# Kernel tuning notes

Hardware: AMD Instinct MI355X
Metric: run time of the kernel (lower is better)

## Reference

```python
import jax, jax.numpy as jnp
import numpy as np

N, K, C, CL = 1024, 32, 64, 128
H = 2 * C  # MLP hidden = 2 * pair channels


def _ln(x, g, b, eps=1e-5):
    m = x.mean(-1, keepdims=True)
    v = jnp.mean(jnp.square(x - m), -1, keepdims=True)
    return (x - m) * jax.lax.rsqrt(v + eps) * g + b


def setup_inputs() -> dict:
    key = jax.random.key(0)
    ks = jax.random.split(key, 16)

    def w(k, shape):
        return jax.random.normal(k, shape, jnp.float32) / np.float32(np.sqrt(shape[0]))

    local = jax.random.normal(ks[0], (N, CL), jnp.float32)
    pair = jax.random.normal(ks[1], (N, N, C), jnp.float32)
    pair_update = jax.random.normal(ks[2], (N, K, C), jnp.float32)
    r = jax.random.randint(ks[3], (N, K), -(N // 4), N)
    neighbours = jnp.where(r < 0, -1, r)
    mask = jax.random.bernoulli(ks[4], 0.9, (N,))
    return dict(
        local=local, pair=pair, pair_update=pair_update,
        neighbours=neighbours, mask=mask,
        Wa=w(ks[5], (CL, C)), Wb=w(ks[6], (CL, C)),
        ln_g=jnp.ones((C,), jnp.float32), ln_b=jnp.zeros((C,), jnp.float32),
        W_aug=w(ks[7], (C, C)), W_lin=w(ks[8], (C, C)),
        W_left=w(ks[9], (C, 32)), b_left=jnp.zeros((32,), jnp.float32),
        W_right=w(ks[10], (C, 32)), b_right=jnp.zeros((32,), jnp.float32),
        W1=w(ks[11], (32, H)), W2=w(ks[12], (H, C)),
        W_int=w(ks[13], (CL, C)), b_int=jnp.zeros((C,), jnp.float32),
    )


def reference(local, pair, pair_update, neighbours, mask,
              Wa, Wb, ln_g, ln_b, W_aug, W_lin,
              W_left, b_left, W_right, b_right, W1, W2, W_int, b_int):
    idx = jnp.arange(pair.shape[0])
    # inject local info into the sparse pair update   [N,K,C]
    pu = pair_update + (local @ Wa)[:, None] + (local @ Wb)[neighbours]
    # gather neighbour pair features + layernorm      [N,K,C]
    lp = _ln(pair[idx[:, None], neighbours], ln_g, ln_b)
    lp = lp + pu @ W_aug
    linear = lp @ W_lin                               # [N,K,C]
    left = lp @ W_left + b_left                       # [N,K,32]
    right = lp @ W_right + b_right                    # [N,K,32]
    # neighbour-of-neighbour pair features            [N,K,K,32]
    npair = left[:, None] + right[neighbours]
    pn = neighbours[neighbours]                       # [N,K,K]
    pn = jnp.where((neighbours == -1)[:, :, None], pn, -1)
    pm = (pn != -1) & mask[pn] & (neighbours != -1)[:, None, :]
    # fused per-edge-pair MLP                          [N,K,K,C]
    upd = jax.nn.gelu(npair @ W1) @ W2
    # masked mean over the middle neighbour axis       [N,K,C]
    upd = jnp.where(pm[..., None], upd, 0.0).sum(axis=1)
    upd = upd / jnp.maximum(pm.sum(axis=1), 1).astype(upd.dtype)[..., None]
    inter = local @ W_int + b_int                     # [N,C]
    # scatter-add back into the dense pair tensor (collisions possible)
    return pair.at[idx[:, None], neighbours].add(upd + inter[:, None] + linear)
```

## Files before the change

### kernel.cpp

```cpp
#include <hip/hip_runtime.h>
#include <hip/hip_bf16.h>

constexpr int Nn  = 1024;
constexpr int Kk  = 32;
constexpr int Cc  = 64;
constexpr int CLl = 128;

typedef unsigned int   u32;
typedef unsigned short u16;
typedef float f4v __attribute__((ext_vector_type(4)));

__device__ __forceinline__ float gelu_tanh(float v){
  float c = 0.7978845608028654f*(v + 0.044715f*v*v*v);
  return 0.5f*v*(1.f + tanhf(c));
}
__device__ __forceinline__ float bflo(u32 u){ return __uint_as_float(u<<16); }
__device__ __forceinline__ float bfhi(u32 u){ return __uint_as_float(u & 0xffff0000u); }
__device__ __forceinline__ u32 pack_bf(float a, float b){
  u32 xa = __float_as_uint(a), xb = __float_as_uint(b);
  u32 ra = (xa + 0x7fffu + ((xa>>16)&1u)) >> 16;
  u32 rb = (xb + 0x7fffu + ((xb>>16)&1u)) >> 16;
  return ra | (rb<<16);
}

__global__ __launch_bounds__(256) void kcopy(
    const f4v* __restrict__ src, f4v* __restrict__ dst,
    const float* __restrict__ local, const float* __restrict__ Wa,
    const float* __restrict__ Wb, const float* __restrict__ Wint,
    const float* __restrict__ b_int,
    float* __restrict__ A, float* __restrict__ B, float* __restrict__ inter){
  const int tid = threadIdx.x;
  size_t base = (size_t)blockIdx.x * (256*32) + tid;
  #pragma unroll
  for(int g = 0; g < 4; ++g){
    f4v v[8];
    #pragma unroll
    for(int j = 0; j < 8; ++j)
      v[j] = __builtin_nontemporal_load(&src[base + (size_t)(g*8 + j)*256]);
    #pragma unroll
    for(int j = 0; j < 8; ++j)
      __builtin_nontemporal_store(v[j], &dst[base + (size_t)(g*8 + j)*256]);
  }
  if(blockIdx.x < (unsigned)Nn){
    __shared__ float l[CLl];
    if(tid < CLl) l[tid] = local[blockIdx.x*CLl + tid];
    __syncthreads();
    if(tid < 64){
      const int c = tid, i = blockIdx.x;
      float a = 0.f, b = 0.f, t = 0.f;
      #pragma unroll 4
      for(int d = 0; d < CLl; ++d){
        float ld = l[d];
        a = fmaf(ld, Wa[d*Cc + c], a);
        b = fmaf(ld, Wb[d*Cc + c], b);
        t = fmaf(ld, Wint[d*Cc + c], t);
      }
      A[i*Cc + c] = a;
      B[i*Cc + c] = b;
      inter[i*Cc + c] = t + b_int[c];
    }
  }
}

__global__ __launch_bounds__(256) void k1(
    const float* __restrict__ pair, const float* __restrict__ pair_update,
    const int* __restrict__ neigh, const int* __restrict__ mask,
    const float* __restrict__ ln_g, const float* __restrict__ ln_b,
    const float* __restrict__ W_aug, const float* __restrict__ W_right,
    const float* __restrict__ b_right,
    const float* __restrict__ A, const float* __restrict__ B,
    float* __restrict__ r1023, int* __restrict__ qpart){
  const int i = Nn - 1;
  __shared__ float wA[4096];
  __shared__ float wR[2048];
  __shared__ float p [Kk][68];
  __shared__ float pu[Kk][68];
  __shared__ float lp[Kk][68];
  __shared__ int   nwS[Kk];
  __shared__ float ssum[Kk][9], ssq[Kk][9], stats[Kk][2];
  int tid = threadIdx.x;
  for(int idx = tid; idx < 4096; idx += 256) wA[idx] = W_aug[idx];
  for(int idx = tid; idx < 2048; idx += 256) wR[idx] = W_right[idx];
  if(tid < Kk){
    int n = neigh[i*Kk + tid];
    nwS[tid] = (n < 0) ? n + Nn : n;
    qpart[tid] = (n != -1 && mask[n] != 0) ? 1 : 0;
  }
  __syncthreads();
  int k = tid >> 3, s = tid & 7;
  {
    const float* prow = pair + ((size_t)i*Nn + nwS[k])*Cc + s*8;
    const float* pur  = pair_update + ((size_t)i*Kk + k)*Cc + s*8;
    const float* Ar = A + i*Cc + s*8;
    const float* Br = B + (size_t)nwS[k]*Cc + s*8;
    float ps = 0.f, ps2 = 0.f;
    for(int j = 0; j < 8; ++j){
      float v = prow[j];
      p[k][s*8 + j] = v; ps += v; ps2 += v*v;
      pu[k][s*8 + j] = pur[j] + Ar[j] + Br[j];
    }
    ssum[k][s] = ps; ssq[k][s] = ps2;
  }
  __syncthreads();
  if(s == 0){
    float m = 0.f, q = 0.f;
    for(int j = 0; j < 8; ++j){ m += ssum[k][j]; q += ssq[k][j]; }
    m *= (1.f/64.f); q *= (1.f/64.f);
    float var = fmaxf(q - m*m, 0.f);
    stats[k][0] = m; stats[k][1] = rsqrtf(var + 1e-5f);
  }
  __syncthreads();
  {
    float m = stats[k][0], r = stats[k][1];
    float acc[8];
    #pragma unroll
    for(int j = 0; j < 8; ++j){
      int c = s*8 + j;
      acc[j] = (p[k][c] - m)*r*ln_g[c] + ln_b[c];
    }
    for(int d = 0; d < 64; ++d){
      float pd = pu[k][d];
      #pragma unroll
      for(int j = 0; j < 8; ++j) acc[j] = fmaf(pd, wA[d*64 + s*8 + j], acc[j]);
    }
    #pragma unroll
    for(int j = 0; j < 8; ++j) lp[k][s*8 + j] = acc[j];
  }
  __syncthreads();
  {
    float acc[4] = {0.f,0.f,0.f,0.f};
    for(int d = 0; d < 64; ++d){
      float ld = lp[k][d];
      #pragma unroll
      for(int j = 0; j < 4; ++j) acc[j] = fmaf(ld, wR[d*32 + s*4 + j], acc[j]);
    }
    #pragma unroll
    for(int j = 0; j < 4; ++j)
      r1023[k*32 + s*4 + j] = acc[j] + b_right[s*4 + j];
  }
}

__global__ __launch_bounds__(256) void kcomp(
    const float* __restrict__ pair, const float* __restrict__ pair_update,
    const int* __restrict__ neigh,
    const float* __restrict__ ln_g, const float* __restrict__ ln_b,
    const float* __restrict__ W_aug, const float* __restrict__ W_lin,
    const float* __restrict__ W_left, const float* __restrict__ b_left,
    const float* __restrict__ W1, const float* __restrict__ W2,
    const float* __restrict__ A, const float* __restrict__ B,
    const float* __restrict__ inter, const float* __restrict__ r1023,
    const int* __restrict__ qpart,
    float* __restrict__ out){

  __shared__ u32 wbA[2048];
  __shared__ u32 wbL[2048];
  __shared__ u32 wbF[1024];
  __shared__ u32 w1b[2048];
  __shared__ u32 w2b[4096];
  __shared__ float pbuf[Kk][68];
  __shared__ u32  puP [Kk][34];
  __shared__ float uA[1088];
  __shared__ float stats[Kk][2];
  __shared__ float AiS[64], InS[64], lgS[64], lbS[64];
  __shared__ int nbS[Kk], nwS[Kk], quS[Kk], leadS[Kk];
  __shared__ int cminus;

  float* ssum = uA;
  float* ssq  = uA + 288;
  float* hbuf = uA;

  const int i   = blockIdx.x;
  const int tid = threadIdx.x;

  for(int idx = tid; idx < 2048; idx += 256){
    const float2 wa = *(const float2*)(W_aug + idx*2);
    wbA[idx] = pack_bf(wa.x, wa.y);
    const float2 wl = *(const float2*)(W_lin + idx*2);
    wbL[idx] = pack_bf(wl.x, wl.y);
    const float2 w1 = *(const float2*)(W1 + idx*2);
    w1b[idx] = pack_bf(w1.x, w1.y);
    const float2 w2a = *(const float2*)(W2 + idx*2);
    w2b[idx] = pack_bf(w2a.x, w2a.y);
    const float2 w2c = *(const float2*)(W2 + 4096 + idx*2);
    w2b[2048 + idx] = pack_bf(w2c.x, w2c.y);
  }
  for(int idx = tid; idx < 1024; idx += 256){
    const float2 wf = *(const float2*)(W_left + idx*2);
    wbF[idx] = pack_bf(wf.x, wf.y);
  }
  if(tid < Kk){
    int n = neigh[i*Kk + tid];
    nbS[tid] = n;
    nwS[tid] = (n < 0) ? n + Nn : n;
    quS[tid] = qpart[tid];
  }
  if(tid < 64){
    AiS[tid] = A[i*Cc + tid];
    InS[tid] = inter[i*Cc + tid];
    lgS[tid] = ln_g[tid];
    lbS[tid] = ln_b[tid];
  }
  __syncthreads();

  if(tid == 0){
    int c = 0;
    for(int kk = 0; kk < Kk; ++kk) c |= (nbS[kk] == -1);
    cminus = c;
  }
  if(tid < Kk){
    int lead = 1;
    for(int kk = 0; kk < tid; ++kk) if(nwS[kk] == nwS[tid]) lead = 0;
    leadS[tid] = lead;
  }

  float pf[8];
  {
    int k8 = tid >> 3, s8 = tid & 7;
    const float4* p4 = (const float4*)(pair + ((size_t)i*Nn + nwS[k8])*Cc) + s8*2;
    float4 p0 = p4[0], p1 = p4[1];
    const float4* u4 = (const float4*)(pair_update + ((size_t)i*Kk + k8)*Cc) + s8*2;
    float4 u0 = u4[0], u1 = u4[1];
    const float4* Br = (const float4*)(B + (size_t)nwS[k8]*Cc) + s8*2;
    float4 b0 = Br[0], b1 = Br[1];
    pf[0]=p0.x; pf[1]=p0.y; pf[2]=p0.z; pf[3]=p0.w;
    pf[4]=p1.x; pf[5]=p1.y; pf[6]=p1.z; pf[7]=p1.w;
    float uf[8] = {u0.x,u0.y,u0.z,u0.w,u1.x,u1.y,u1.z,u1.w};
    float bv[8] = {b0.x,b0.y,b0.z,b0.w,b1.x,b1.y,b1.z,b1.w};
    float ps = 0.f, ps2 = 0.f;
    #pragma unroll
    for(int j = 0; j < 8; ++j){
      float v = pf[j];
      pbuf[k8][s8*8 + j] = v; ps += v; ps2 += v*v;
    }
    #pragma unroll
    for(int j = 0; j < 4; ++j){
      float e0 = uf[2*j]   + AiS[s8*8 + 2*j]   + bv[2*j];
      float e1 = uf[2*j+1] + AiS[s8*8 + 2*j+1] + bv[2*j+1];
      puP[k8][s8*4 + j] = pack_bf(e0, e1);
    }
    ssum[k8*9 + s8] = ps; ssq[k8*9 + s8] = ps2;
  }
  __syncthreads();

  if((tid & 7) == 0){
    int k8 = tid >> 3;
    float m = 0.f, q = 0.f;
    for(int j = 0; j < 8; ++j){ m += ssum[k8*9 + j]; q += ssq[k8*9 + j]; }
    m *= (1.f/64.f); q *= (1.f/64.f);
    float var = fmaxf(q - m*m, 0.f);
    stats[k8][0] = m; stats[k8][1] = rsqrtf(var + 1e-5f);
  }
  __syncthreads();

  const int kq  = tid >> 4;
  const int s   = tid & 15;
  const int k0i = kq, k1i = kq + 16;
  const int c0  = s*4;

  float a0[4], a1[4];
  {
    float m0 = stats[k0i][0], r0 = stats[k0i][1];
    float m1 = stats[k1i][0], r1 = stats[k1i][1];
    #pragma unroll
    for(int j = 0; j < 4; ++j){
      int c = c0 + j;
      a0[j] = (pbuf[k0i][c] - m0)*r0*lgS[c] + lbS[c];
      a1[j] = (pbuf[k1i][c] - m1)*r1*lgS[c] + lbS[c];
    }
    #pragma unroll 2
    for(int dp = 0; dp < 32; ++dp){
      u32 q0 = puP[k0i][dp], q1 = puP[k1i][dp];
      float pe0 = bflo(q0), po0 = bfhi(q0);
      float pe1 = bflo(q1), po1 = bfhi(q1);
      uint2 we = *(const uint2*)&wbA[(2*dp)*32 + s*2];
      uint2 wo = *(const uint2*)&wbA[(2*dp+1)*32 + s*2];
      float w0 = bflo(we.x), w1 = bfhi(we.x), w2 = bflo(we.y), w3 = bfhi(we.y);
      a0[0] = fmaf(pe0, w0, a0[0]); a0[1] = fmaf(pe0, w1, a0[1]);
      a0[2] = fmaf(pe0, w2, a0[2]); a0[3] = fmaf(pe0, w3, a0[3]);
      a1[0] = fmaf(pe1, w0, a1[0]); a1[1] = fmaf(pe1, w1, a1[1]);
      a1[2] = fmaf(pe1, w2, a1[2]); a1[3] = fmaf(pe1, w3, a1[3]);
      float x0w = bflo(wo.x), x1w = bfhi(wo.x), x2w = bflo(wo.y), x3w = bfhi(wo.y);
      a0[0] = fmaf(po0, x0w, a0[0]); a0[1] = fmaf(po0, x1w, a0[1]);
      a0[2] = fmaf(po0, x2w, a0[2]); a0[3] = fmaf(po0, x3w, a0[3]);
      a1[0] = fmaf(po1, x0w, a1[0]); a1[1] = fmaf(po1, x1w, a1[1]);
      a1[2] = fmaf(po1, x2w, a1[2]); a1[3] = fmaf(po1, x3w, a1[3]);
    }
  }
  __syncthreads();
  #pragma unroll
  for(int j = 0; j < 4; ++j){ pbuf[k0i][c0 + j] = a0[j]; pbuf[k1i][c0 + j] = a1[j]; }
  __syncthreads();

  float L0[4], L1[4];
  {
    float Lx0[4] = {0,0,0,0}, Lx1[4] = {0,0,0,0};
    float X0[2] = {0,0}, X1[2] = {0,0};
    #pragma unroll 4
    for(int d = 0; d < 64; ++d){
      float p0 = pbuf[k0i][d], p1 = pbuf[k1i][d];
      uint2 wv = *(const uint2*)&wbL[d*32 + s*2];
      float w0 = bflo(wv.x), w1 = bfhi(wv.x), w2 = bflo(wv.y), w3 = bfhi(wv.y);
      Lx0[0] = fmaf(p0, w0, Lx0[0]); Lx0[1] = fmaf(p0, w1, Lx0[1]);
      Lx0[2] = fmaf(p0, w2, Lx0[2]); Lx0[3] = fmaf(p0, w3, Lx0[3]);
      Lx1[0] = fmaf(p1, w0, Lx1[0]); Lx1[1] = fmaf(p1, w1, Lx1[1]);
      Lx1[2] = fmaf(p1, w2, Lx1[2]); Lx1[3] = fmaf(p1, w3, Lx1[3]);
      u32 wf = wbF[d*16 + s];
      float f0 = bflo(wf), f1 = bfhi(wf);
      X0[0] = fmaf(p0, f0, X0[0]); X0[1] = fmaf(p0, f1, X0[1]);
      X1[0] = fmaf(p1, f0, X1[0]); X1[1] = fmaf(p1, f1, X1[1]);
    }
    #pragma unroll
    for(int j = 0; j < 4; ++j){
      L0[j] = Lx0[j] + InS[c0 + j];
      L1[j] = Lx1[j] + InS[c0 + j];
    }
    int x0 = s*2;
    float2 bl = *(const float2*)(b_left + x0);
    float2 rA = *(const float2*)(r1023 + k0i*32 + x0);
    float2 rB = *(const float2*)(r1023 + k1i*32 + x0);
    hbuf[k0i*34 + x0]     = X0[0] + bl.x + rA.x;
    hbuf[k0i*34 + x0 + 1] = X0[1] + bl.y + rA.y;
    hbuf[k1i*34 + x0]     = X1[0] + bl.x + rB.x;
    hbuf[k1i*34 + x0 + 1] = X1[1] + bl.y + rB.y;
  }
  __syncthreads();

  float g0[8], g1v[8];
  {
    float A0[8] = {0,0,0,0,0,0,0,0}, A1[8] = {0,0,0,0,0,0,0,0};
    #pragma unroll 2
    for(int x = 0; x < 32; ++x){
      float h0 = hbuf[k0i*34 + x], h1 = hbuf[k1i*34 + x];
      uint4 wv = *(const uint4*)&w1b[x*64 + s*4];
      float w[8] = {bflo(wv.x),bfhi(wv.x),bflo(wv.y),bfhi(wv.y),
                    bflo(wv.z),bfhi(wv.z),bflo(wv.w),bfhi(wv.w)};
      #pragma unroll
      for(int j = 0; j < 8; ++j){
        A0[j] = fmaf(h0, w[j], A0[j]);
        A1[j] = fmaf(h1, w[j], A1[j]);
      }
    }
    #pragma unroll
    for(int j = 0; j < 8; ++j){ g0[j] = gelu_tanh(A0[j]); g1v[j] = gelu_tanh(A1[j]); }
  }
  {
    float V0[4] = {0,0,0,0}, V1[4] = {0,0,0,0};
    int lbase = (kq & 3) << 4;
    for(int hb = 0; hb < 16; ++hb){
      int srcl = lbase | hb;
      #pragma unroll
      for(int hj = 0; hj < 8; ++hj){
        float gA = __shfl(g0[hj],  srcl, 64);
        float gB = __shfl(g1v[hj], srcl, 64);
        int h = hb*8 + hj;
        uint2 wv = *(const uint2*)&w2b[h*32 + s*2];
        float w0 = bflo(wv.x), w1 = bfhi(wv.x), w2 = bflo(wv.y), w3 = bfhi(wv.y);
        V0[0] = fmaf(gA, w0, V0[0]); V0[1] = fmaf(gA, w1, V0[1]);
        V0[2] = fmaf(gA, w2, V0[2]); V0[3] = fmaf(gA, w3, V0[3]);
        V1[0] = fmaf(gB, w0, V1[0]); V1[1] = fmaf(gB, w1, V1[1]);
        V1[2] = fmaf(gB, w2, V1[2]); V1[3] = fmaf(gB, w3, V1[3]);
      }
    }
    float mul0 = (cminus && quS[k0i] && nbS[k0i] != -1) ? 1.f : 0.f;
    float mul1 = (cminus && quS[k1i] && nbS[k1i] != -1) ? 1.f : 0.f;
    #pragma unroll
    for(int j = 0; j < 4; ++j){
      pbuf[k0i][c0 + j] = fmaf(mul0, V0[j], L0[j]);
      pbuf[k1i][c0 + j] = fmaf(mul1, V1[j], L1[j]);
    }
  }
  __syncthreads();

  {
    int k8 = tid >> 3, s8 = tid & 7;
    if(leadS[k8]){
      int col = nwS[k8];
      float tot[8] = {0,0,0,0,0,0,0,0};
      for(int kk = 0; kk < Kk; ++kk){
        if(nwS[kk] == col){
          #pragma unroll
          for(int j = 0; j < 8; ++j) tot[j] += pbuf[kk][s8*8 + j];
        }
      }
      size_t base = ((size_t)i*Nn + col)*Cc + s8*8;
      float4 o0 = make_float4(pf[0]+tot[0], pf[1]+tot[1], pf[2]+tot[2], pf[3]+tot[3]);
      float4 o1 = make_float4(pf[4]+tot[4], pf[5]+tot[5], pf[6]+tot[6], pf[7]+tot[7]);
      float4* ov = (float4*)(out + base);
      ov[0] = o0; ov[1] = o1;
    }
  }
}

extern "C" void kernel_launch(void* const* d_in, const int* in_sizes, int n_in,
                              void* d_out, int out_size, void* d_ws, size_t ws_size,
                              hipStream_t stream){
  (void)in_sizes; (void)n_in; (void)out_size; (void)ws_size;
  const float* local       = (const float*)d_in[0];
  const float* pair        = (const float*)d_in[1];
  const float* pair_update = (const float*)d_in[2];
  const int*   neighbours  = (const int*)d_in[3];
  const int*   mask        = (const int*)d_in[4];
  const float* Wa          = (const float*)d_in[5];
  const float* Wb          = (const float*)d_in[6];
  const float* ln_g        = (const float*)d_in[7];
  const float* ln_b        = (const float*)d_in[8];
  const float* W_aug       = (const float*)d_in[9];
  const float* W_lin       = (const float*)d_in[10];
  const float* W_left      = (const float*)d_in[11];
  const float* b_left      = (const float*)d_in[12];
  const float* W_right     = (const float*)d_in[13];
  const float* b_right     = (const float*)d_in[14];
  const float* W1          = (const float*)d_in[15];
  const float* W2          = (const float*)d_in[16];
  const float* W_int       = (const float*)d_in[17];
  const float* b_int       = (const float*)d_in[18];

  float* ws    = (float*)d_ws;
  float* A     = ws;
  float* B     = ws + 65536;
  float* inter = ws + 131072;
  float* r1023 = ws + 196608;
  int*   qpart = (int*)(ws + 197632);

  kcopy<<<dim3(2048), dim3(256), 0, stream>>>(
      (const f4v*)pair, (f4v*)d_out,
      local, Wa, Wb, W_int, b_int, A, B, inter);
  k1<<<dim3(1), dim3(256), 0, stream>>>(pair, pair_update, neighbours, mask,
                                        ln_g, ln_b, W_aug, W_right, b_right,
                                        A, B, r1023, qpart);
  kcomp<<<dim3(Nn), dim3(256), 0, stream>>>(pair, pair_update, neighbours,
                                            ln_g, ln_b, W_aug, W_lin,
                                            W_left, b_left, W1, W2,
                                            A, B, inter, r1023, qpart,
                                            (float*)d_out);
}
```

Before: 540.5 us.

## Alias kcomp weight LDS buffers for occupancy and split copy kernel

Result: slower. 558.4 us (+3.3%).

```diff
diff --git a/kernel.cpp b/kernel.cpp
--- a/kernel.cpp
+++ b/kernel.cpp
@@ -23,43 +23,28 @@
   return ra | (rb<<16);
 }
 
-__global__ __launch_bounds__(256) void kcopy(
-    const f4v* __restrict__ src, f4v* __restrict__ dst,
+__global__ __launch_bounds__(64) void k0(
     const float* __restrict__ local, const float* __restrict__ Wa,
     const float* __restrict__ Wb, const float* __restrict__ Wint,
     const float* __restrict__ b_int,
     float* __restrict__ A, float* __restrict__ B, float* __restrict__ inter){
-  const int tid = threadIdx.x;
-  size_t base = (size_t)blockIdx.x * (256*32) + tid;
-  #pragma unroll
-  for(int g = 0; g < 4; ++g){
-    f4v v[8];
-    #pragma unroll
-    for(int j = 0; j < 8; ++j)
-      v[j] = __builtin_nontemporal_load(&src[base + (size_t)(g*8 + j)*256]);
-    #pragma unroll
-    for(int j = 0; j < 8; ++j)
-      __builtin_nontemporal_store(v[j], &dst[base + (size_t)(g*8 + j)*256]);
-  }
-  if(blockIdx.x < (unsigned)Nn){
-    __shared__ float l[CLl];
-    if(tid < CLl) l[tid] = local[blockIdx.x*CLl + tid];
-    __syncthreads();
-    if(tid < 64){
-      const int c = tid, i = blockIdx.x;
-      float a = 0.f, b = 0.f, t = 0.f;
-      #pragma unroll 4
-      for(int d = 0; d < CLl; ++d){
-        float ld = l[d];
-        a = fmaf(ld, Wa[d*Cc + c], a);
-        b = fmaf(ld, Wb[d*Cc + c], b);
-        t = fmaf(ld, Wint[d*Cc + c], t);
-      }
-      A[i*Cc + c] = a;
-      B[i*Cc + c] = b;
-      inter[i*Cc + c] = t + b_int[c];
-    }
-  }
+  int i = blockIdx.x;
+  int c = threadIdx.x;
+  __shared__ float l[CLl];
+  l[c]      = local[i*CLl + c];
+  l[c + 64] = local[i*CLl + 64 + c];
+  __syncthreads();
+  float a = 0.f, b = 0.f, t = 0.f;
+  #pragma unroll 4
+  for(int d = 0; d < CLl; ++d){
+    float ld = l[d];
+    a = fmaf(ld, Wa[d*Cc + c], a);
+    b = fmaf(ld, Wb[d*Cc + c], b);
+    t = fmaf(ld, Wint[d*Cc + c], t);
+  }
+  A[i*Cc + c] = a;
+  B[i*Cc + c] = b;
+  inter[i*Cc + c] = t + b_int[c];
 }
 
 __global__ __launch_bounds__(256) void k1(
@@ -140,7 +125,21 @@
   }
 }
 
-__global__ __launch_bounds__(256) void kcomp(
+__global__ __launch_bounds__(256) void kcopy(
+    const f4v* __restrict__ src, f4v* __restrict__ dst){
+  const int tid = threadIdx.x;
+  size_t base = (size_t)blockIdx.x * (256*32) + tid;
+  #pragma unroll
+  for(int g = 0; g < 4; ++g){
+    f4v v[8];
+    #pragma unroll
+    for(int j = 0; j < 8; ++j) v[j] = src[base + (size_t)(g*8 + j)*256];
+    #pragma unroll
+    for(int j = 0; j < 8; ++j) dst[base + (size_t)(g*8 + j)*256] = v[j];
+  }
+}
+
+__global__ __launch_bounds__(256, 3) void kcomp(
     const float* __restrict__ pair, const float* __restrict__ pair_update,
     const int* __restrict__ neigh,
     const float* __restrict__ ln_g, const float* __restrict__ ln_b,
@@ -152,11 +151,7 @@
     const int* __restrict__ qpart,
     float* __restrict__ out){
 
-  __shared__ u32 wbA[2048];
-  __shared__ u32 wbL[2048];
-  __shared__ u32 wbF[1024];
-  __shared__ u32 w1b[2048];
-  __shared__ u32 w2b[4096];
+  __shared__ u32 wreg[6144];
   __shared__ float pbuf[Kk][68];
   __shared__ u32  puP [Kk][34];
   __shared__ float uA[1088];
@@ -165,6 +160,12 @@
   __shared__ int nbS[Kk], nwS[Kk], quS[Kk], leadS[Kk];
   __shared__ int cminus;
 
+  u32* wbA = wreg;
+  u32* wbL = wreg + 2048;
+  u32* wbF = wreg + 4096;
+  u32* w1b = wreg;
+  u32* w2b = wreg + 2048;
+
   float* ssum = uA;
   float* ssq  = uA + 288;
   float* hbuf = uA;
@@ -177,12 +178,6 @@
     wbA[idx] = pack_bf(wa.x, wa.y);
     const float2 wl = *(const float2*)(W_lin + idx*2);
     wbL[idx] = pack_bf(wl.x, wl.y);
-    const float2 w1 = *(const float2*)(W1 + idx*2);
-    w1b[idx] = pack_bf(w1.x, w1.y);
-    const float2 w2a = *(const float2*)(W2 + idx*2);
-    w2b[idx] = pack_bf(w2a.x, w2a.y);
-    const float2 w2c = *(const float2*)(W2 + 4096 + idx*2);
-    w2b[2048 + idx] = pack_bf(w2c.x, w2c.y);
   }
   for(int idx = tid; idx < 1024; idx += 256){
     const float2 wf = *(const float2*)(W_left + idx*2);
@@ -322,6 +317,16 @@
     hbuf[k0i*34 + x0 + 1] = X0[1] + bl.y + rA.y;
     hbuf[k1i*34 + x0]     = X1[0] + bl.x + rB.x;
     hbuf[k1i*34 + x0 + 1] = X1[1] + bl.y + rB.y;
+  }
+  __syncthreads();
+
+  for(int idx = tid; idx < 2048; idx += 256){
+    const float2 w1 = *(const float2*)(W1 + idx*2);
+    w1b[idx] = pack_bf(w1.x, w1.y);
+    const float2 w2a = *(const float2*)(W2 + idx*2);
+    w2b[idx] = pack_bf(w2a.x, w2a.y);
+    const float2 w2c = *(const float2*)(W2 + 4096 + idx*2);
+    w2b[2048 + idx] = pack_bf(w2c.x, w2c.y);
   }
   __syncthreads();
 
@@ -422,12 +427,11 @@
   float* r1023 = ws + 196608;
   int*   qpart = (int*)(ws + 197632);
 
-  kcopy<<<dim3(2048), dim3(256), 0, stream>>>(
-      (const f4v*)pair, (f4v*)d_out,
-      local, Wa, Wb, W_int, b_int, A, B, inter);
+  k0<<<dim3(Nn), dim3(64), 0, stream>>>(local, Wa, Wb, W_int, b_int, A, B, inter);
   k1<<<dim3(1), dim3(256), 0, stream>>>(pair, pair_update, neighbours, mask,
                                         ln_g, ln_b, W_aug, W_right, b_right,
                                         A, B, r1023, qpart);
+  kcopy<<<dim3(2048), dim3(256), 0, stream>>>((const f4v*)pair, (f4v*)d_out);
   kcomp<<<dim3(Nn), dim3(256), 0, stream>>>(pair, pair_update, neighbours,
                                             ln_g, ln_b, W_aug, W_lin,
                                             W_left, b_left, W1, W2,
```
